# Kernel tuning notes

Measured on AMD Instinct MI355X. Metric: run time of the kernel, lower is better.

## Reference

```python
import jax, jax.numpy as jnp
import numpy as np

B, S, D, H = 2, 2048, 1024, 16
DK = D // H


def setup_inputs() -> dict:
    key = jax.random.key(0)
    ks = jax.random.split(key, 12)
    sc = 0.02
    inp = {
        "q": jax.random.normal(ks[0], (B, S, D), jnp.float32),
        "k": jax.random.normal(ks[1], (B, S, D), jnp.float32),
        "v": jax.random.normal(ks[2], (B, S, D), jnp.float32),
        "mask": jnp.ones((B, S, S), jnp.int32),
        "Wq": jax.random.normal(ks[3], (D, D), jnp.float32) * sc,
        "bq": jnp.zeros((D,), jnp.float32),
        "Wk": jax.random.normal(ks[4], (D, D), jnp.float32) * sc,
        "bk": jnp.zeros((D,), jnp.float32),
        "Wv": jax.random.normal(ks[5], (D, D), jnp.float32) * sc,
        "bv": jnp.zeros((D,), jnp.float32),
        "Wo": jax.random.normal(ks[6], (D, D), jnp.float32) * sc,
        "bo": jnp.zeros((D,), jnp.float32),
    }
    return inp


def _split_heads(x):
    # [B,S,D] -> [B,H,S,DK]
    b, s, _ = x.shape
    return x.reshape(b, s, H, DK).transpose(0, 2, 1, 3)


def reference(q, k, v, mask, Wq, bq, Wk, bk, Wv, bv, Wo, bo):
    qh = _split_heads(q @ Wq.T + bq)
    kh = _split_heads(k @ Wk.T + bk)
    vh = _split_heads(v @ Wv.T + bv)
    scale = 1.0 / jnp.sqrt(jnp.float32(DK))
    scores = jnp.einsum("bhqd,bhkd->bhqk", qh, kh) * scale  # [B,H,S,S]
    scores = jnp.where(mask[:, None, :, :] == 0, jnp.float32(-1e9), scores)
    probs = jax.nn.softmax(scores, axis=-1)  # dropout p=0.0 -> identity
    out = jnp.einsum("bhqk,bhkd->bhqd", probs, vh)  # [B,H,S,DK]
    concat = out.transpose(0, 2, 1, 3).reshape(q.shape[0], -1, D)
    return concat @ Wo.T + bo
```

## Files before the change

### kernel.cpp

```cpp
#include <hip/hip_runtime.h>
#include <stdint.h>

#define Bsz 2
#define Ssz 2048
#define Dsz 1024
#define Hsz 16
#define DKsz 64

typedef __attribute__((ext_vector_type(8))) short sh8;
typedef __attribute__((ext_vector_type(4))) float fx4;
typedef __attribute__((ext_vector_type(16))) float fx16;
typedef __attribute__((ext_vector_type(4))) unsigned ux4;

__device__ __forceinline__ unsigned short f2bf(float x) {
  uint32_t u = __builtin_bit_cast(uint32_t, x);
  uint32_t r = (u + 0x7fffu + ((u >> 16) & 1u)) >> 16;
  return (unsigned short)r;
}

__device__ __forceinline__ fx4 mfma16(sh8 a, sh8 b, fx4 c) {
  return __builtin_amdgcn_mfma_f32_16x16x32_bf16(a, b, c, 0, 0, 0);
}

__device__ __forceinline__ fx16 mfma32(sh8 a, sh8 b, fx16 c) {
  return __builtin_amdgcn_mfma_f32_32x32x16_bf16(a, b, c, 0, 0, 0);
}

__device__ __forceinline__ void g2l16(const void* g, void* l) {
  __builtin_amdgcn_global_load_lds((const __attribute__((address_space(1))) void*)g,
                                   (__attribute__((address_space(3))) void*)l, 16, 0, 0);
}

__device__ __forceinline__ float fexp2(float x) {
#if __has_builtin(__builtin_amdgcn_exp2f)
  return __builtin_amdgcn_exp2f(x);
#else
  return exp2f(x);
#endif
}

__device__ __forceinline__ unsigned cvtpk(float lo, float hi) {
  unsigned r;
  asm("v_cvt_pk_bf16_f32 %0, %1, %2" : "=v"(r) : "v"(lo), "v"(hi));
  return r;
}

__device__ __forceinline__ void plswap(unsigned& a, unsigned& b) {
  asm("v_permlane32_swap_b32 %0, %1" : "+v"(a), "+v"(b));
}

__device__ __forceinline__ void build_pa(const fx16& p, sh8& pa0, sh8& pa1) {
  unsigned w0 = cvtpk(p[0], p[1]), w1 = cvtpk(p[2], p[3]);
  unsigned w2 = cvtpk(p[4], p[5]), w3 = cvtpk(p[6], p[7]);
  unsigned w4 = cvtpk(p[8], p[9]), w5 = cvtpk(p[10], p[11]);
  unsigned w6 = cvtpk(p[12], p[13]), w7 = cvtpk(p[14], p[15]);
  plswap(w0, w2);
  plswap(w1, w3);
  ux4 u0 = {w0, w1, w2, w3};
  pa0 = __builtin_bit_cast(sh8, u0);
  plswap(w4, w6);
  plswap(w5, w7);
  ux4 u1 = {w4, w5, w6, w7};
  pa1 = __builtin_bit_cast(sh8, u1);
}

__global__ __launch_bounds__(256) void convert_kernel(
    const float* __restrict__ q, const float* __restrict__ k, const float* __restrict__ v,
    const float* __restrict__ wq, const float* __restrict__ wk, const float* __restrict__ wv,
    const float* __restrict__ wo, const int* __restrict__ mask,
    unsigned short* __restrict__ qb, unsigned short* __restrict__ kb, unsigned short* __restrict__ vb,
    unsigned short* __restrict__ wqb, unsigned short* __restrict__ wkb, unsigned short* __restrict__ wvb,
    unsigned short* __restrict__ wob, int* __restrict__ flag) {
  const int NQ = Bsz * Ssz * Dsz / 4;
  const int NW = Dsz * Dsz / 4;
  const int NC = 3 * NQ + 4 * NW;
  const int NM = Bsz * Ssz * Ssz / 4;
  const int total = NC + NM;
  int bad = 0;
  for (int i = blockIdx.x * blockDim.x + threadIdx.x; i < total; i += gridDim.x * blockDim.x) {
    if (i >= NC) {
      int4 m = ((const int4*)mask)[i - NC];
      if (m.x == 0 || m.y == 0 || m.z == 0 || m.w == 0) bad = 1;
      continue;
    }
    const float* src; unsigned short* dst; int off;
    if (i < 3 * NQ) {
      int t = i / NQ; off = i - t * NQ;
      src = (t == 0) ? q : ((t == 1) ? k : v);
      dst = (t == 0) ? qb : ((t == 1) ? kb : vb);
    } else {
      int j = i - 3 * NQ; int t = j / NW; off = j - t * NW;
      src = (t == 0) ? wq : ((t == 1) ? wk : ((t == 2) ? wv : wo));
      dst = (t == 0) ? wqb : ((t == 1) ? wkb : ((t == 2) ? wvb : wob));
    }
    float4 x = ((const float4*)src)[off];
    ushort4 o;
    o.x = f2bf(x.x); o.y = f2bf(x.y); o.z = f2bf(x.z); o.w = f2bf(x.w);
    ((ushort4*)dst)[off] = o;
  }
  if (bad) atomicAnd(flag, 0);
}

__global__ void flag_init_kernel(int* flag) {
  if (threadIdx.x == 0 && blockIdx.x == 0) flag[0] = 1;
}

__global__ __launch_bounds__(256) void proj_qkv_kernel(
    const unsigned short* __restrict__ qb, const unsigned short* __restrict__ kb,
    const unsigned short* __restrict__ vb,
    const unsigned short* __restrict__ wqb, const unsigned short* __restrict__ wkb,
    const unsigned short* __restrict__ wvb,
    const float* __restrict__ bq, const float* __restrict__ bk, const float* __restrict__ bv,
    unsigned short* __restrict__ qh, unsigned short* __restrict__ kh,
    unsigned short* __restrict__ vt) {
  __shared__ __align__(16) unsigned short As[128 * 32];
  __shared__ __align__(16) unsigned short Bs[128 * 32];
  __shared__ __align__(16) unsigned short Ts[128 * 136];
  const int z = blockIdx.z;
  const unsigned short* X = (z == 0) ? qb : ((z == 1) ? kb : vb);
  const unsigned short* W = (z == 0) ? wqb : ((z == 1) ? wkb : wvb);
  const float* bias = (z == 0) ? bq : ((z == 1) ? bk : bv);
  const int m0 = blockIdx.x * 128, n0 = blockIdx.y * 128;
  const int tid = threadIdx.x, lane = tid & 63, wid = tid >> 6;
  const int wm = wid >> 1, wn = wid & 1;
  const int c = lane & 15, g = lane >> 4;
  fx4 acc[4][4] = {};
  for (int k0 = 0; k0 < Dsz; k0 += 32) {
#pragma unroll
    for (int i = 0; i < 2; i++) {
      int e = i * 256 + tid;
      g2l16(X + (size_t)(m0 + (e >> 2)) * Dsz + k0 + (e & 3) * 8,
            (char*)As + (size_t)(i * 256 + wid * 64) * 16);
      g2l16(W + (size_t)(n0 + (e >> 2)) * Dsz + k0 + (e & 3) * 8,
            (char*)Bs + (size_t)(i * 256 + wid * 64) * 16);
    }
    __syncthreads();
    sh8 af[4], bfr[4];
#pragma unroll
    for (int m = 0; m < 4; m++)
      af[m] = *(const sh8*)&As[(wm * 64 + m * 16 + c) * 32 + g * 8];
#pragma unroll
    for (int n = 0; n < 4; n++)
      bfr[n] = *(const sh8*)&Bs[(wn * 64 + n * 16 + c) * 32 + g * 8];
#pragma unroll
    for (int m = 0; m < 4; m++)
#pragma unroll
      for (int n = 0; n < 4; n++)
        acc[m][n] = mfma16(af[m], bfr[n], acc[m][n]);
    __syncthreads();
  }
  if (z < 2) {
    unsigned short* O = (z == 0) ? qh : kh;
#pragma unroll
    for (int n = 0; n < 4; n++) {
      int j = n0 + wn * 64 + n * 16 + c;
      float bj = bias[j];
      int h = j >> 6, dk = j & 63;
#pragma unroll
      for (int m = 0; m < 4; m++)
#pragma unroll
        for (int r = 0; r < 4; r++) {
          int i = m0 + wm * 64 + m * 16 + g * 4 + r;
          int b = i >> 11, s = i & 2047;
          O[(((size_t)(b * Hsz + h) * Ssz + s) << 6) + dk] = f2bf(acc[m][n][r] + bj);
        }
    }
  } else {
#pragma unroll
    for (int n = 0; n < 4; n++) {
      int nl = wn * 64 + n * 16 + c;
      float bj = bias[n0 + nl];
#pragma unroll
      for (int m = 0; m < 4; m++)
#pragma unroll
        for (int r = 0; r < 4; r++) {
          int ml = wm * 64 + m * 16 + g * 4 + r;
          Ts[nl * 136 + ml] = f2bf(acc[m][n][r] + bj);
        }
    }
    __syncthreads();
    int b = m0 >> 11, sbase = m0 & 2047;
#pragma unroll
    for (int it = 0; it < 8; it++) {
      int ch = it * 256 + tid;
      int row = ch >> 4, off = ch & 15;
      sh8 dv = *(const sh8*)&Ts[row * 136 + off * 8];
      int j = n0 + row;
      int h = j >> 6, dk = j & 63;
      *(sh8*)&vt[(size_t)((b * Hsz + h) * DKsz + dk) * Ssz + sbase + off * 8] = dv;
    }
  }
}

__global__ __launch_bounds__(512, 4) void attn_kernel(
    const unsigned short* __restrict__ qh, const unsigned short* __restrict__ kh,
    const unsigned short* __restrict__ vt, const int* __restrict__ mask,
    const int* __restrict__ flag, unsigned short* __restrict__ concat) {
  __shared__ __align__(16) unsigned short SM[2][2][2][4096];
  const int tid = threadIdx.x, lane = tid & 63, wid = tid >> 6;
  const int grp = wid >> 2, w4 = wid & 3;
  const int fid = blockIdx.y * gridDim.x + blockIdx.x;
  const int logical = (fid & 7) * 64 + (fid >> 3);
  const int bh = logical >> 4, qblk = logical & 15;
  const int b = bh >> 4, h = bh & 15;
  const int q0 = qblk * 128 + w4 * 32;
  const int c = lane & 31, hi = lane >> 5;
  const int cs = c & 7;
  const int kvbase = grp * (Ssz / 2);
  const unsigned short* Qb = qh + ((size_t)bh * Ssz + q0) * DKsz;
  const unsigned short* Kb = kh + (size_t)bh * Ssz * DKsz;
  const unsigned short* Vb = vt + (size_t)bh * DKsz * Ssz;
  const int ch0 = w4 * 128 + lane;
  const int ch1 = ch0 + 64;
  const int r0 = ch0 >> 3, sl0 = (ch0 & 7) ^ (r0 & 7);
  const int r1 = ch1 >> 3, sl1 = (ch1 & 7) ^ (r1 & 7);
  const int koff0 = r0 * DKsz + sl0 * 8, koff1 = r1 * DKsz + sl1 * 8;
  const size_t voff0 = (size_t)r0 * Ssz + sl0 * 8, voff1 = (size_t)r1 * Ssz + sl1 * 8;

  sh8 qf[4];
#pragma unroll
  for (int ks = 0; ks < 4; ks++)
    qf[ks] = *(const sh8*)&Qb[(size_t)c * DKsz + ks * 16 + hi * 8];
  const bool allones = (flag[0] != 0);
  const float CE = 0.18033688011112042f;
  float lsum = 0.f;
  fx16 o0 = {}, o1 = {};

  auto STAGE = [&](int bufi, int kv0) {
    const unsigned short* ksrc = Kb + (size_t)kv0 * DKsz;
    char* kdst = (char*)&SM[0][grp][bufi][0] + w4 * 2048;
    g2l16(ksrc + koff0, kdst);
    g2l16(ksrc + koff1, kdst + 1024);
    const unsigned short* vsrc = Vb + kv0;
    char* vdst = (char*)&SM[1][grp][bufi][0] + w4 * 2048;
    g2l16(vsrc + voff0, vdst);
    g2l16(vsrc + voff1, vdst + 1024);
  };

  const int NT = (Ssz / 2) / 64;
  STAGE(0, kvbase);
  asm volatile("s_waitcnt vmcnt(0)" ::: "memory");
  __builtin_amdgcn_s_barrier();
  asm volatile("" ::: "memory");

  for (int t = 0; t < NT; ++t) {
    const int cur = t & 1;
    const int kv0 = kvbase + t * 64;
    if (t + 1 < NT) STAGE(cur ^ 1, kv0 + 64);
    const unsigned short* Kt = &SM[0][grp][cur][0];
    const unsigned short* Vt = &SM[1][grp][cur][0];
    fx16 s0 = {}, s1 = {};
    __builtin_amdgcn_s_setprio(1);
#pragma unroll
    for (int ks = 0; ks < 4; ks++) {
      int sl = (2 * ks + hi) ^ cs;
      sh8 ka = *(const sh8*)&Kt[(c * 8 + sl) * 8];
      sh8 kb2 = *(const sh8*)&Kt[((32 + c) * 8 + sl) * 8];
      s0 = mfma32(ka, qf[ks], s0);
      s1 = mfma32(kb2, qf[ks], s1);
    }
    __builtin_amdgcn_s_setprio(0);
    if (!allones) {
      const int* mrow = mask + ((size_t)b * Ssz + (q0 + c)) * Ssz + kv0;
#pragma unroll
      for (int r = 0; r < 16; r++) {
        int kv = (r & 3) + 8 * (r >> 2) + 4 * hi;
        if (mrow[kv] == 0) s0[r] = -1e9f;
        if (mrow[32 + kv] == 0) s1[r] = -1e9f;
      }
    }
    fx16 p0v, p1v;
#pragma unroll
    for (int r = 0; r < 16; r++) {
      p0v[r] = fexp2(s0[r] * CE);
      p1v[r] = fexp2(s1[r] * CE);
    }
    sh8 pa[4];
    build_pa(p0v, pa[0], pa[1]);
    build_pa(p1v, pa[2], pa[3]);
    __builtin_amdgcn_s_setprio(1);
#pragma unroll
    for (int ks = 0; ks < 4; ks++) {
      int sl = (2 * ks + hi) ^ cs;
      sh8 v0f = *(const sh8*)&Vt[(c * 8 + sl) * 8];
      sh8 v1f = *(const sh8*)&Vt[((32 + c) * 8 + sl) * 8];
      o0 = mfma32(v0f, pa[ks], o0);
      o1 = mfma32(v1f, pa[ks], o1);
    }
    __builtin_amdgcn_s_setprio(0);
    float sm[16];
#pragma unroll
    for (int r = 0; r < 16; r++) sm[r] = p0v[r] + p1v[r];
#pragma unroll
    for (int w = 8; w >= 1; w >>= 1)
#pragma unroll
      for (int r = 0; r < w; r++) sm[r] += sm[r + w];
    lsum += sm[0];
    asm volatile("s_waitcnt vmcnt(0)" ::: "memory");
    __builtin_amdgcn_s_barrier();
    asm volatile("" ::: "memory");
  }

  float* CB = (float*)&SM[0][0][0][0];
  float* CBl = CB + 4 * 32 * 68;
  if (grp == 1) {
#pragma unroll
    for (int k4 = 0; k4 < 4; k4++) {
      fx4 a = {o0[4 * k4], o0[4 * k4 + 1], o0[4 * k4 + 2], o0[4 * k4 + 3]};
      *(fx4*)&CB[(w4 * 32 + c) * 68 + 8 * k4 + 4 * hi] = a;
      fx4 bvv = {o1[4 * k4], o1[4 * k4 + 1], o1[4 * k4 + 2], o1[4 * k4 + 3]};
      *(fx4*)&CB[(w4 * 32 + c) * 68 + 32 + 8 * k4 + 4 * hi] = bvv;
    }
    CBl[w4 * 64 + hi * 32 + c] = lsum;
  }
  __syncthreads();
  if (grp == 0) {
#pragma unroll
    for (int k4 = 0; k4 < 4; k4++) {
      fx4 a = *(const fx4*)&CB[(w4 * 32 + c) * 68 + 8 * k4 + 4 * hi];
      o0[4 * k4] += a[0]; o0[4 * k4 + 1] += a[1]; o0[4 * k4 + 2] += a[2]; o0[4 * k4 + 3] += a[3];
      fx4 bvv = *(const fx4*)&CB[(w4 * 32 + c) * 68 + 32 + 8 * k4 + 4 * hi];
      o1[4 * k4] += bvv[0]; o1[4 * k4 + 1] += bvv[1]; o1[4 * k4 + 2] += bvv[2]; o1[4 * k4 + 3] += bvv[3];
    }
    lsum += CBl[w4 * 64 + hi * 32 + c];
    lsum += __shfl_xor(lsum, 32);
    float linv = 1.0f / lsum;
    unsigned short* Ob = concat + ((size_t)b * Ssz + q0 + c) * Dsz + h * DKsz;
#pragma unroll
    for (int rg = 0; rg < 4; rg++) {
      ushort4 w;
      w.x = f2bf(o0[rg * 4 + 0] * linv);
      w.y = f2bf(o0[rg * 4 + 1] * linv);
      w.z = f2bf(o0[rg * 4 + 2] * linv);
      w.w = f2bf(o0[rg * 4 + 3] * linv);
      *(ushort4*)&Ob[8 * rg + 4 * hi] = w;
      ushort4 w2;
      w2.x = f2bf(o1[rg * 4 + 0] * linv);
      w2.y = f2bf(o1[rg * 4 + 1] * linv);
      w2.z = f2bf(o1[rg * 4 + 2] * linv);
      w2.w = f2bf(o1[rg * 4 + 3] * linv);
      *(ushort4*)&Ob[32 + 8 * rg + 4 * hi] = w2;
    }
  }
}

__global__ __launch_bounds__(256) void outproj_kernel(
    const unsigned short* __restrict__ Xc, const unsigned short* __restrict__ wob,
    const float* __restrict__ bo, float* __restrict__ out) {
  __shared__ __align__(16) unsigned short As[128 * 32];
  __shared__ __align__(16) unsigned short Bs[128 * 32];
  const int m0 = blockIdx.x * 128, n0 = blockIdx.y * 128;
  const int tid = threadIdx.x, lane = tid & 63, wid = tid >> 6;
  const int wm = wid >> 1, wn = wid & 1;
  const int c = lane & 15, g = lane >> 4;
  fx4 acc[4][4] = {};
  for (int k0 = 0; k0 < Dsz; k0 += 32) {
#pragma unroll
    for (int i = 0; i < 2; i++) {
      int e = i * 256 + tid;
      g2l16(Xc + (size_t)(m0 + (e >> 2)) * Dsz + k0 + (e & 3) * 8,
            (char*)As + (size_t)(i * 256 + wid * 64) * 16);
      g2l16(wob + (size_t)(n0 + (e >> 2)) * Dsz + k0 + (e & 3) * 8,
            (char*)Bs + (size_t)(i * 256 + wid * 64) * 16);
    }
    __syncthreads();
    sh8 af[4], bfr[4];
#pragma unroll
    for (int m = 0; m < 4; m++)
      af[m] = *(const sh8*)&As[(wm * 64 + m * 16 + c) * 32 + g * 8];
#pragma unroll
    for (int n = 0; n < 4; n++)
      bfr[n] = *(const sh8*)&Bs[(wn * 64 + n * 16 + c) * 32 + g * 8];
#pragma unroll
    for (int m = 0; m < 4; m++)
#pragma unroll
      for (int n = 0; n < 4; n++)
        acc[m][n] = mfma16(af[m], bfr[n], acc[m][n]);
    __syncthreads();
  }
#pragma unroll
  for (int n = 0; n < 4; n++) {
    int j = n0 + wn * 64 + n * 16 + c;
    float bj = bo[j];
#pragma unroll
    for (int m = 0; m < 4; m++)
#pragma unroll
      for (int r = 0; r < 4; r++) {
        int i = m0 + wm * 64 + m * 16 + g * 4 + r;
        out[(size_t)i * Dsz + j] = acc[m][n][r] + bj;
      }
  }
}

extern "C" void kernel_launch(void* const* d_in, const int* in_sizes, int n_in,
                              void* d_out, int out_size, void* d_ws, size_t ws_size,
                              hipStream_t stream) {
  const float* q = (const float*)d_in[0];
  const float* k = (const float*)d_in[1];
  const float* v = (const float*)d_in[2];
  const int* mask = (const int*)d_in[3];
  const float* Wq = (const float*)d_in[4];
  const float* bq = (const float*)d_in[5];
  const float* Wk = (const float*)d_in[6];
  const float* bk = (const float*)d_in[7];
  const float* Wv = (const float*)d_in[8];
  const float* bv = (const float*)d_in[9];
  const float* Wo = (const float*)d_in[10];
  const float* bo = (const float*)d_in[11];
  float* out = (float*)d_out;
  char* ws = (char*)d_ws;
  const size_t MB = 1 << 20;
  unsigned short* qb  = (unsigned short*)(ws + 0 * MB);
  unsigned short* kb  = (unsigned short*)(ws + 8 * MB);
  unsigned short* vb  = (unsigned short*)(ws + 16 * MB);
  unsigned short* wqb = (unsigned short*)(ws + 24 * MB);
  unsigned short* wkb = (unsigned short*)(ws + 26 * MB);
  unsigned short* wvb = (unsigned short*)(ws + 28 * MB);
  unsigned short* wob = (unsigned short*)(ws + 30 * MB);
  unsigned short* qhp = (unsigned short*)(ws + 32 * MB);
  unsigned short* khp = (unsigned short*)(ws + 40 * MB);
  unsigned short* vtp = (unsigned short*)(ws + 48 * MB);
  unsigned short* cc  = (unsigned short*)(ws + 56 * MB);
  int* flag = (int*)(ws + 64 * MB);

  hipLaunchKernelGGL(flag_init_kernel, dim3(1), dim3(64), 0, stream, flag);
  hipLaunchKernelGGL(convert_kernel, dim3(2048), dim3(256), 0, stream,
                     q, k, v, Wq, Wk, Wv, Wo, mask, qb, kb, vb, wqb, wkb, wvb, wob, flag);
  hipLaunchKernelGGL(proj_qkv_kernel, dim3(32, 8, 3), dim3(256), 0, stream,
                     qb, kb, vb, wqb, wkb, wvb, bq, bk, bv, qhp, khp, vtp);
  hipLaunchKernelGGL(attn_kernel, dim3(16, 32), dim3(512), 0, stream,
                     qhp, khp, vtp, mask, flag, cc);
  hipLaunchKernelGGL(outproj_kernel, dim3(32, 8), dim3(256), 0, stream,
                     cc, wob, bo, out);
}
```

Measured before the change: 147.4 us.

## Fuse fp32-to-bf16 activation conversion into QKV projection with double-buffered LDS

The separate conversion of q/k/v activations to bf16 is removed. The projection kernel now loads fp32 activations directly, converts them in registers and writes them to double-buffered shared memory, overlapping the next tile's loads with the current compute. The softmax exp2 scale is also folded into the Q projection epilogue, which removes a multiply per score in attention. This avoids a full write and re-read of the activations to global memory, at the cost of more register pressure and twice as many bytes loaded per activation tile.

```diff
diff --git a/kernel.cpp b/kernel.cpp
--- a/kernel.cpp
+++ b/kernel.cpp
@@ -65,15 +65,13 @@
 }
 
 __global__ __launch_bounds__(256) void convert_kernel(
-    const float* __restrict__ q, const float* __restrict__ k, const float* __restrict__ v,
     const float* __restrict__ wq, const float* __restrict__ wk, const float* __restrict__ wv,
     const float* __restrict__ wo, const int* __restrict__ mask,
-    unsigned short* __restrict__ qb, unsigned short* __restrict__ kb, unsigned short* __restrict__ vb,
-    unsigned short* __restrict__ wqb, unsigned short* __restrict__ wkb, unsigned short* __restrict__ wvb,
-    unsigned short* __restrict__ wob, int* __restrict__ flag) {
-  const int NQ = Bsz * Ssz * Dsz / 4;
+    unsigned short* __restrict__ wqb, unsigned short* __restrict__ wkb,
+    unsigned short* __restrict__ wvb, unsigned short* __restrict__ wob,
+    int* __restrict__ flag) {
   const int NW = Dsz * Dsz / 4;
-  const int NC = 3 * NQ + 4 * NW;
+  const int NC = 4 * NW;
   const int NM = Bsz * Ssz * Ssz / 4;
   const int total = NC + NM;
   int bad = 0;
@@ -83,16 +81,9 @@
       if (m.x == 0 || m.y == 0 || m.z == 0 || m.w == 0) bad = 1;
       continue;
     }
-    const float* src; unsigned short* dst; int off;
-    if (i < 3 * NQ) {
-      int t = i / NQ; off = i - t * NQ;
-      src = (t == 0) ? q : ((t == 1) ? k : v);
-      dst = (t == 0) ? qb : ((t == 1) ? kb : vb);
-    } else {
-      int j = i - 3 * NQ; int t = j / NW; off = j - t * NW;
-      src = (t == 0) ? wq : ((t == 1) ? wk : ((t == 2) ? wv : wo));
-      dst = (t == 0) ? wqb : ((t == 1) ? wkb : ((t == 2) ? wvb : wob));
-    }
+    int t = i / NW, off = i - t * NW;
+    const float* src = (t == 0) ? wq : ((t == 1) ? wk : ((t == 2) ? wv : wo));
+    unsigned short* dst = (t == 0) ? wqb : ((t == 1) ? wkb : ((t == 2) ? wvb : wob));
     float4 x = ((const float4*)src)[off];
     ushort4 o;
     o.x = f2bf(x.x); o.y = f2bf(x.y); o.z = f2bf(x.z); o.w = f2bf(x.w);
@@ -106,18 +97,20 @@
 }
 
 __global__ __launch_bounds__(256) void proj_qkv_kernel(
-    const unsigned short* __restrict__ qb, const unsigned short* __restrict__ kb,
-    const unsigned short* __restrict__ vb,
+    const float* __restrict__ qf, const float* __restrict__ kf, const float* __restrict__ vf,
     const unsigned short* __restrict__ wqb, const unsigned short* __restrict__ wkb,
     const unsigned short* __restrict__ wvb,
     const float* __restrict__ bq, const float* __restrict__ bk, const float* __restrict__ bv,
     unsigned short* __restrict__ qh, unsigned short* __restrict__ kh,
     unsigned short* __restrict__ vt) {
-  __shared__ __align__(16) unsigned short As[128 * 32];
-  __shared__ __align__(16) unsigned short Bs[128 * 32];
-  __shared__ __align__(16) unsigned short Ts[128 * 136];
+  __shared__ __align__(16) unsigned short SMEM[17408];
+  unsigned short* As0 = SMEM;
+  unsigned short* As1 = SMEM + 4096;
+  unsigned short* Bs0 = SMEM + 8192;
+  unsigned short* Bs1 = SMEM + 12288;
+  unsigned short* Ts = SMEM;
   const int z = blockIdx.z;
-  const unsigned short* X = (z == 0) ? qb : ((z == 1) ? kb : vb);
+  const float* X = (z == 0) ? qf : ((z == 1) ? kf : vf);
   const unsigned short* W = (z == 0) ? wqb : ((z == 1) ? wkb : wvb);
   const float* bias = (z == 0) ? bq : ((z == 1) ? bk : bv);
   const int m0 = blockIdx.x * 128, n0 = blockIdx.y * 128;
@@ -125,16 +118,33 @@
   const int wm = wid >> 1, wn = wid & 1;
   const int c = lane & 15, g = lane >> 4;
   fx4 acc[4][4] = {};
-  for (int k0 = 0; k0 < Dsz; k0 += 32) {
+
+  auto LOADA = [&](int k0, float4* a) {
+#pragma unroll
+    for (int i = 0; i < 4; i++) {
+      int c4 = i * 256 + tid;
+      a[i] = *(const float4*)(X + (size_t)(m0 + (c4 >> 3)) * Dsz + k0 + (c4 & 7) * 4);
+    }
+  };
+  auto WRITEA = [&](const float4* a, unsigned short* As) {
+#pragma unroll
+    for (int i = 0; i < 4; i++) {
+      int c4 = i * 256 + tid;
+      uint2 w;
+      w.x = cvtpk(a[i].x, a[i].y);
+      w.y = cvtpk(a[i].z, a[i].w);
+      *(uint2*)&As[(c4 >> 3) * 32 + (c4 & 7) * 4] = w;
+    }
+  };
+  auto G2LB = [&](int k0, unsigned short* Bs) {
 #pragma unroll
     for (int i = 0; i < 2; i++) {
       int e = i * 256 + tid;
-      g2l16(X + (size_t)(m0 + (e >> 2)) * Dsz + k0 + (e & 3) * 8,
-            (char*)As + (size_t)(i * 256 + wid * 64) * 16);
       g2l16(W + (size_t)(n0 + (e >> 2)) * Dsz + k0 + (e & 3) * 8,
             (char*)Bs + (size_t)(i * 256 + wid * 64) * 16);
     }
-    __syncthreads();
+  };
+  auto COMPUTE = [&](const unsigned short* As, const unsigned short* Bs) {
     sh8 af[4], bfr[4];
 #pragma unroll
     for (int m = 0; m < 4; m++)
@@ -147,10 +157,30 @@
 #pragma unroll
       for (int n = 0; n < 4; n++)
         acc[m][n] = mfma16(af[m], bfr[n], acc[m][n]);
+  };
+
+  float4 aA[4], aB[4];
+  LOADA(0, aA);
+  G2LB(0, Bs0);
+  WRITEA(aA, As0);
+  __syncthreads();
+#pragma unroll 1
+  for (int j = 0; j < 16; j++) {
+    const int k0 = j * 64;
+    if (k0 + 32 < Dsz) { LOADA(k0 + 32, aB); G2LB(k0 + 32, Bs1); }
+    COMPUTE(As0, Bs0);
+    if (k0 + 32 < Dsz) WRITEA(aB, As1);
     __syncthreads();
-  }
+    if (k0 + 64 < Dsz) { LOADA(k0 + 64, aA); G2LB(k0 + 64, Bs0); }
+    if (k0 + 32 < Dsz) COMPUTE(As1, Bs1);
+    if (k0 + 64 < Dsz) WRITEA(aA, As0);
+    __syncthreads();
+  }
+
+  const float CE = 0.18033688011112042f;
   if (z < 2) {
     unsigned short* O = (z == 0) ? qh : kh;
+    const float sc = (z == 0) ? CE : 1.0f;
 #pragma unroll
     for (int n = 0; n < 4; n++) {
       int j = n0 + wn * 64 + n * 16 + c;
@@ -162,7 +192,7 @@
         for (int r = 0; r < 4; r++) {
           int i = m0 + wm * 64 + m * 16 + g * 4 + r;
           int b = i >> 11, s = i & 2047;
-          O[(((size_t)(b * Hsz + h) * Ssz + s) << 6) + dk] = f2bf(acc[m][n][r] + bj);
+          O[(((size_t)(b * Hsz + h) * Ssz + s) << 6) + dk] = f2bf((acc[m][n][r] + bj) * sc);
         }
     }
   } else {
@@ -222,7 +252,6 @@
   for (int ks = 0; ks < 4; ks++)
     qf[ks] = *(const sh8*)&Qb[(size_t)c * DKsz + ks * 16 + hi * 8];
   const bool allones = (flag[0] != 0);
-  const float CE = 0.18033688011112042f;
   float lsum = 0.f;
   fx16 o0 = {}, o1 = {};
 
@@ -272,8 +301,8 @@
     fx16 p0v, p1v;
 #pragma unroll
     for (int r = 0; r < 16; r++) {
-      p0v[r] = fexp2(s0[r] * CE);
-      p1v[r] = fexp2(s1[r] * CE);
+      p0v[r] = fexp2(s0[r]);
+      p1v[r] = fexp2(s1[r]);
     }
     sh8 pa[4];
     build_pa(p0v, pa[0], pa[1]);
@@ -410,24 +439,21 @@
   float* out = (float*)d_out;
   char* ws = (char*)d_ws;
   const size_t MB = 1 << 20;
-  unsigned short* qb  = (unsigned short*)(ws + 0 * MB);
-  unsigned short* kb  = (unsigned short*)(ws + 8 * MB);
-  unsigned short* vb  = (unsigned short*)(ws + 16 * MB);
-  unsigned short* wqb = (unsigned short*)(ws + 24 * MB);
-  unsigned short* wkb = (unsigned short*)(ws + 26 * MB);
-  unsigned short* wvb = (unsigned short*)(ws + 28 * MB);
-  unsigned short* wob = (unsigned short*)(ws + 30 * MB);
-  unsigned short* qhp = (unsigned short*)(ws + 32 * MB);
-  unsigned short* khp = (unsigned short*)(ws + 40 * MB);
-  unsigned short* vtp = (unsigned short*)(ws + 48 * MB);
-  unsigned short* cc  = (unsigned short*)(ws + 56 * MB);
-  int* flag = (int*)(ws + 64 * MB);
+  unsigned short* wqb = (unsigned short*)(ws + 0 * MB);
+  unsigned short* wkb = (unsigned short*)(ws + 2 * MB);
+  unsigned short* wvb = (unsigned short*)(ws + 4 * MB);
+  unsigned short* wob = (unsigned short*)(ws + 6 * MB);
+  unsigned short* qhp = (unsigned short*)(ws + 8 * MB);
+  unsigned short* khp = (unsigned short*)(ws + 16 * MB);
+  unsigned short* vtp = (unsigned short*)(ws + 24 * MB);
+  unsigned short* cc  = (unsigned short*)(ws + 32 * MB);
+  int* flag = (int*)(ws + 40 * MB);
 
   hipLaunchKernelGGL(flag_init_kernel, dim3(1), dim3(64), 0, stream, flag);
-  hipLaunchKernelGGL(convert_kernel, dim3(2048), dim3(256), 0, stream,
-                     q, k, v, Wq, Wk, Wv, Wo, mask, qb, kb, vb, wqb, wkb, wvb, wob, flag);
+  hipLaunchKernelGGL(convert_kernel, dim3(1024), dim3(256), 0, stream,
+                     Wq, Wk, Wv, Wo, mask, wqb, wkb, wvb, wob, flag);
   hipLaunchKernelGGL(proj_qkv_kernel, dim3(32, 8, 3), dim3(256), 0, stream,
-                     qb, kb, vb, wqb, wkb, wvb, bq, bk, bv, qhp, khp, vtp);
+                     q, k, v, wqb, wkb, wvb, bq, bk, bv, qhp, khp, vtp);
   hipLaunchKernelGGL(attn_kernel, dim3(16, 32), dim3(512), 0, stream,
                      qhp, khp, vtp, mask, flag, cc);
   hipLaunchKernelGGL(outproj_kernel, dim3(32, 8), dim3(256), 0, stream,
```

After: 139.1 us. 5.6% less time.
